# Kernel tuning notes

Measured on AMD Instinct MI355X. Metric: run time of the kernel, lower is better.

## Reference

```python
import jax, jax.numpy as jnp
import numpy as np


def setup_inputs() -> dict:
    key = jax.random.key(0)
    x = jax.random.normal(key, (16, 512, 512, 8), dtype=jnp.float32)
    # 3x3 structuring element with center False: neighbors-only local max
    mask = jnp.array([[True, True, True],
                      [True, False, True],
                      [True, True, True]])
    return {"x": x, "mask": mask}


def reference(x, mask):
    # Equivalent of tf.nn.dilation2d(x, where(mask, 0, -inf), SAME, stride 1):
    # masked_max[b,i,j,c] = max over (di,dj) in mask of x[b,i+di-ph, j+dj-pw, c]
    # (out-of-bounds treated as -inf, matching dilation's identity padding).
    kh, kw = mask.shape  # small static window (e.g. 3x3)
    H, W = x.shape[1], x.shape[2]
    ph, pw = (kh - 1) // 2, (kw - 1) // 2
    neg_inf = jnp.asarray(-jnp.inf, x.dtype)
    xp = jnp.pad(x, ((0, 0), (ph, kh - 1 - ph), (pw, kw - 1 - pw), (0, 0)),
                 constant_values=-np.inf)
    masked_max = jnp.full_like(x, -np.inf)
    for di in range(kh):          # fixed small kernel loop (9 taps), not a data-dim loop
        for dj in range(kw):
            win = xp[:, di:di + H, dj:dj + W, :]
            masked_max = jnp.maximum(masked_max, jnp.where(mask[di, dj], win, neg_inf))
    # suppressed = cast(x > masked_max) * x
    return (x > masked_max).astype(x.dtype) * x
```

## Files before the change

### kernel.cpp

```cpp
#include <hip/hip_runtime.h>
#include <math.h>


constexpr int Hdim = 512;
constexpr int Wdim = 512;
constexpr int HPT  = 8;
constexpr int ROWS = HPT + 2;
constexpr int ROW  = Wdim * 2;

__device__ __forceinline__ float4 f4max(float4 a, float4 b) {
    return make_float4(fmaxf(a.x,b.x), fmaxf(a.y,b.y), fmaxf(a.z,b.z), fmaxf(a.w,b.w));
}

__global__ __launch_bounds__(256) void nms_kernel(
    const float4* __restrict__ x,
    const unsigned char* __restrict__ mask_bytes,
    float4* __restrict__ out)
{
    const int* mi = (const int*)mask_bytes;
    bool intlay = true;
    #pragma unroll
    for (int i = 0; i < 9; ++i) { int v = mi[i]; intlay = intlay && (v == 0 || v == 1); }
    bool m[9];
    #pragma unroll
    for (int i = 0; i < 9; ++i) m[i] = intlay ? (mi[i] != 0) : (mask_bytes[i] != 0);

    int gid = blockIdx.x * blockDim.x + threadIdx.x;
    int c4 = gid & 1;
    int w  = (gid >> 1) & (Wdim - 1);
    int hg = (gid >> 10) & 63;
    int n  = gid >> 16;
    int h0 = hg * HPT;

    const float4 NEG = make_float4(-INFINITY, -INFINITY, -INFINITY, -INFINITY);
    bool aok = (w > 0), cok = (w < Wdim - 1);
    int ao = aok ? -2 : 0;
    int co = cok ?  2 : 0;

    int base = ((n * Hdim + h0) * Wdim + w) * 2 + c4;

    float4 A[ROWS], B[ROWS], C[ROWS];
    #pragma unroll
    for (int r = 0; r < ROWS; ++r) {
        int hr = h0 - 1 + r;
        int hc = hr < 0 ? 0 : (hr > Hdim - 1 ? Hdim - 1 : hr);
        int rb = base + (hc - h0) * ROW;
        A[r] = x[rb + ao];
        B[r] = x[rb];
        C[r] = x[rb + co];
    }

    bool topclamp = (h0 == 0);
    bool botclamp = (h0 + HPT == Hdim);

    #pragma unroll
    for (int s = 0; s < HPT; ++s) {
        bool r0ok = !(s == 0 && topclamp);
        bool r2ok = !(s == HPT - 1 && botclamp);

        float4 va = NEG, vb = NEG, vc = NEG;
        if (m[0] && r0ok) va = f4max(va, A[s]);
        if (m[3])         va = f4max(va, A[s + 1]);
        if (m[6] && r2ok) va = f4max(va, A[s + 2]);
        if (m[1] && r0ok) vb = f4max(vb, B[s]);
        if (m[4])         vb = f4max(vb, B[s + 1]);
        if (m[7] && r2ok) vb = f4max(vb, B[s + 2]);
        if (m[2] && r0ok) vc = f4max(vc, C[s]);
        if (m[5])         vc = f4max(vc, C[s + 1]);
        if (m[8] && r2ok) vc = f4max(vc, C[s + 2]);

        va.x = aok ? va.x : -INFINITY; va.y = aok ? va.y : -INFINITY;
        va.z = aok ? va.z : -INFINITY; va.w = aok ? va.w : -INFINITY;
        vc.x = cok ? vc.x : -INFINITY; vc.y = cok ? vc.y : -INFINITY;
        vc.z = cok ? vc.z : -INFINITY; vc.w = cok ? vc.w : -INFINITY;

        float4 mm = f4max(f4max(va, vb), vc);
        float4 ctr = B[s + 1];
        float4 o;
        o.x = (ctr.x > mm.x) ? ctr.x : 0.0f;
        o.y = (ctr.y > mm.y) ? ctr.y : 0.0f;
        o.z = (ctr.z > mm.z) ? ctr.z : 0.0f;
        o.w = (ctr.w > mm.w) ? ctr.w : 0.0f;
        out[base + s * ROW] = o;
    }
}

extern "C" void kernel_launch(void* const* d_in, const int* in_sizes, int n_in,
                              void* d_out, int out_size, void* d_ws, size_t ws_size,
                              hipStream_t stream) {
    const float4* x = (const float4*)d_in[0];
    const unsigned char* mask = (const unsigned char*)d_in[1];
    float4* out = (float4*)d_out;

    int total = 16 * (Hdim / HPT) * Wdim * 2;
    int block = 256;
    int grid = total / block;
    nms_kernel<<<grid, block, 0, stream>>>(x, mask, out);
}
```

Baseline: 232.1 us.

## Stage row tiles with halo in LDS instead of triple global loads

Each block now loads a 10-row by 260-float4 tile, including a horizontal halo padded with -inf, into shared memory once. Threads then read their left, center and right neighbours from LDS rather than issuing three global loads per row. Boundary handling moves into the load phase, which removes the per-row clamp predicates in the compute loop. The cost is a __syncthreads, about 41KB of LDS per block that may limit occupancy, and extra halo loads handled by a few threads.

```diff
diff --git a/kernel.cpp b/kernel.cpp
--- a/kernel.cpp
+++ b/kernel.cpp
@@ -6,10 +6,16 @@
 constexpr int Wdim = 512;
 constexpr int HPT  = 8;
 constexpr int ROWS = HPT + 2;
-constexpr int ROW  = Wdim * 2;
+constexpr int GPB  = 256;
+constexpr int HALO = 2;
+constexpr int LW   = GPB + 2 * HALO;
+constexpr int ROWG = Wdim * 2;
 
 __device__ __forceinline__ float4 f4max(float4 a, float4 b) {
     return make_float4(fmaxf(a.x,b.x), fmaxf(a.y,b.y), fmaxf(a.z,b.z), fmaxf(a.w,b.w));
+}
+__device__ __forceinline__ float4 f4sel(bool ok, float4 v, float4 e) {
+    return make_float4(ok ? v.x : e.x, ok ? v.y : e.y, ok ? v.z : e.z, ok ? v.w : e.w);
 }
 
 __global__ __launch_bounds__(256) void nms_kernel(
@@ -17,6 +23,8 @@
     const unsigned char* __restrict__ mask_bytes,
     float4* __restrict__ out)
 {
+    __shared__ float4 lds[ROWS][LW];
+
     const int* mi = (const int*)mask_bytes;
     bool intlay = true;
     #pragma unroll
@@ -25,63 +33,70 @@
     #pragma unroll
     for (int i = 0; i < 9; ++i) m[i] = intlay ? (mi[i] != 0) : (mask_bytes[i] != 0);
 
-    int gid = blockIdx.x * blockDim.x + threadIdx.x;
-    int c4 = gid & 1;
-    int w  = (gid >> 1) & (Wdim - 1);
-    int hg = (gid >> 10) & 63;
-    int n  = gid >> 16;
-    int h0 = hg * HPT;
+    const float4 NEG = make_float4(-INFINITY, -INFINITY, -INFINITY, -INFINITY);
 
-    const float4 NEG = make_float4(-INFINITY, -INFINITY, -INFINITY, -INFINITY);
-    bool aok = (w > 0), cok = (w < Wdim - 1);
-    int ao = aok ? -2 : 0;
-    int co = cok ?  2 : 0;
+    int t   = threadIdx.x;
+    int bid = blockIdx.x;
+    int gb  = bid & 3;
+    int hg  = (bid >> 2) & 63;
+    int n   = bid >> 8;
+    int g0  = gb * GPB;
+    int h0  = hg * HPT;
 
-    int base = ((n * Hdim + h0) * Wdim + w) * 2 + c4;
-
-    float4 A[ROWS], B[ROWS], C[ROWS];
     #pragma unroll
     for (int r = 0; r < ROWS; ++r) {
-        int hr = h0 - 1 + r;
-        int hc = hr < 0 ? 0 : (hr > Hdim - 1 ? Hdim - 1 : hr);
-        int rb = base + (hc - h0) * ROW;
-        A[r] = x[rb + ao];
-        B[r] = x[rb];
-        C[r] = x[rb + co];
+        int hr  = h0 - 1 + r;
+        int hrc = hr < 0 ? 0 : (hr > Hdim - 1 ? Hdim - 1 : hr);
+        bool hok = (hr == hrc);
+        long rowbase = ((long)(n * Hdim + hrc)) * ROWG;
+        {
+            int gc  = g0 - HALO + t;
+            int gcc = gc < 0 ? 0 : (gc > ROWG - 1 ? ROWG - 1 : gc);
+            float4 v = x[rowbase + gcc];
+            lds[r][t] = f4sel(hok && (gc == gcc), v, NEG);
+        }
+        if (t < 2 * HALO) {
+            int c   = GPB + t;
+            int gc  = g0 - HALO + c;
+            int gcc = gc < 0 ? 0 : (gc > ROWG - 1 ? ROWG - 1 : gc);
+            float4 v = x[rowbase + gcc];
+            lds[r][c] = f4sel(hok && (gc == gcc), v, NEG);
+        }
     }
+    __syncthreads();
 
-    bool topclamp = (h0 == 0);
-    bool botclamp = (h0 + HPT == Hdim);
+    float4 A0 = lds[0][t], B0 = lds[0][t + 2], C0 = lds[0][t + 4];
+    float4 A1 = lds[1][t], B1 = lds[1][t + 2], C1 = lds[1][t + 4];
+
+    long obase = ((long)(n * Hdim + h0)) * ROWG + g0 + t;
 
     #pragma unroll
     for (int s = 0; s < HPT; ++s) {
-        bool r0ok = !(s == 0 && topclamp);
-        bool r2ok = !(s == HPT - 1 && botclamp);
+        float4 A2 = lds[s + 2][t], B2 = lds[s + 2][t + 2], C2 = lds[s + 2][t + 4];
 
         float4 va = NEG, vb = NEG, vc = NEG;
-        if (m[0] && r0ok) va = f4max(va, A[s]);
-        if (m[3])         va = f4max(va, A[s + 1]);
-        if (m[6] && r2ok) va = f4max(va, A[s + 2]);
-        if (m[1] && r0ok) vb = f4max(vb, B[s]);
-        if (m[4])         vb = f4max(vb, B[s + 1]);
-        if (m[7] && r2ok) vb = f4max(vb, B[s + 2]);
-        if (m[2] && r0ok) vc = f4max(vc, C[s]);
-        if (m[5])         vc = f4max(vc, C[s + 1]);
-        if (m[8] && r2ok) vc = f4max(vc, C[s + 2]);
-
-        va.x = aok ? va.x : -INFINITY; va.y = aok ? va.y : -INFINITY;
-        va.z = aok ? va.z : -INFINITY; va.w = aok ? va.w : -INFINITY;
-        vc.x = cok ? vc.x : -INFINITY; vc.y = cok ? vc.y : -INFINITY;
-        vc.z = cok ? vc.z : -INFINITY; vc.w = cok ? vc.w : -INFINITY;
+        if (m[0]) va = f4max(va, A0);
+        if (m[3]) va = f4max(va, A1);
+        if (m[6]) va = f4max(va, A2);
+        if (m[1]) vb = f4max(vb, B0);
+        if (m[4]) vb = f4max(vb, B1);
+        if (m[7]) vb = f4max(vb, B2);
+        if (m[2]) vc = f4max(vc, C0);
+        if (m[5]) vc = f4max(vc, C1);
+        if (m[8]) vc = f4max(vc, C2);
 
         float4 mm = f4max(f4max(va, vb), vc);
-        float4 ctr = B[s + 1];
+        float4 ctr = B1;
         float4 o;
         o.x = (ctr.x > mm.x) ? ctr.x : 0.0f;
         o.y = (ctr.y > mm.y) ? ctr.y : 0.0f;
         o.z = (ctr.z > mm.z) ? ctr.z : 0.0f;
         o.w = (ctr.w > mm.w) ? ctr.w : 0.0f;
-        out[base + s * ROW] = o;
+        out[obase + s * ROWG] = o;
+
+        A0 = A1; A1 = A2;
+        B0 = B1; B1 = B2;
+        C0 = C1; C1 = C2;
     }
 }
 
@@ -92,8 +107,6 @@
     const unsigned char* mask = (const unsigned char*)d_in[1];
     float4* out = (float4*)d_out;
 
-    int total = 16 * (Hdim / HPT) * Wdim * 2;
-    int block = 256;
-    int grid = total / block;
-    nms_kernel<<<grid, block, 0, stream>>>(x, mask, out);
+    int grid = 16 * (Hdim / HPT) * (ROWG / GPB);
+    nms_kernel<<<grid, 256, 0, stream>>>(x, mask, out);
 }
```

Measured after the change: 267.8 us. 1.15x slower.
